# Performance work log

Measured on AMD Instinct MI355X. Metric: run time of the kernel, lower is better.

The kernel has to match this reference:

```python
import jax, jax.numpy as jnp
import numpy as np

B, S, H = 4, 2048, 768
ROUTING_GAIN = 1.0
LN_EPS = 1e-5
MAS_EPS = 1e-9


def _mas_normalize(logits):
    m = jnp.max(jnp.abs(logits), axis=-1, keepdims=True)
    return jax.nn.relu(logits / (m + MAS_EPS))


def _layer_norm(x, w, b):
    mu = jnp.mean(x, axis=-1, keepdims=True)
    var = jnp.var(x, axis=-1, keepdims=True)
    return (x - mu) / jnp.sqrt(var + LN_EPS) * w + b


def _spl(x, proto, gate, mu_w, mu_b):
    # SparseProtoLinear: comp = x @ mu_w.T + mu_b ; match = x @ proto.T / sqrt(d_in) ; gate_logit = x @ gate.T
    scale = 1.0 / jnp.sqrt(jnp.asarray(x.shape[-1], x.dtype))
    match = jnp.einsum('bsd,od->bso', x, proto) * scale
    gate_logit = jnp.einsum('bsd,od->bso', x, gate)
    comp = jnp.einsum('bsd,od->bso', x, mu_w) + mu_b
    return comp, match, gate_logit


def _gate_branch(inp, comp, match, gate_logit):
    routing_logits = (match - _mas_normalize(gate_logit)) * ROUTING_GAIN
    return (inp + comp) * _mas_normalize(routing_logits)


def _rotate_half(x):
    x1, x2 = jnp.split(x, 2, axis=-1)
    return jnp.concatenate([-x2, x1], axis=-1)


def _apply_rope(q, k, cos, sin):
    return q * cos + _rotate_half(q) * sin, k * cos + _rotate_half(k) * sin


def _causal_attention(q, k, v):
    # single-head SDPA over full hidden dim, causal
    d = q.shape[-1]
    scores = jnp.einsum('bqd,bkd->bqk', q, k) / jnp.sqrt(jnp.asarray(d, q.dtype))
    mask = jnp.tril(jnp.ones((q.shape[1], k.shape[1]), dtype=bool))
    scores = jnp.where(mask, scores, jnp.asarray(-jnp.inf, scores.dtype))
    p = jax.nn.softmax(scores, axis=-1)
    return jnp.einsum('bqk,bkd->bqd', p, v)


def setup_inputs() -> dict:
    key = jax.random.key(0)
    ks = iter(jax.random.split(key, 32))
    w_std = 1.0 / np.sqrt(H)
    inp = {'x': jax.random.normal(next(ks), (B, S, H), jnp.float32)}
    # rotary tables: half-dim frequencies duplicated to full hidden dim
    inv_freq = 1.0 / (10000.0 ** (np.arange(0, H, 2, dtype=np.float32) / H))
    ang = np.arange(S, dtype=np.float32)[:, None] * inv_freq[None, :]  # [S, H/2]
    ang = np.concatenate([ang, ang], axis=-1)  # [S, H]
    inp['cos'] = jnp.asarray(np.cos(ang))
    inp['sin'] = jnp.asarray(np.sin(ang))
    inp['ln1_w'] = jnp.ones((H,), jnp.float32)
    inp['ln1_b'] = jnp.zeros((H,), jnp.float32)
    inp['ln2_w'] = jnp.ones((H,), jnp.float32)
    inp['ln2_b'] = jnp.zeros((H,), jnp.float32)
    for name in ['q', 'k', 'v', 'o', 'f1', 'f2']:
        inp[f'{name}_proto'] = jax.random.normal(next(ks), (H, H), jnp.float32) * w_std
        inp[f'{name}_gate'] = jax.random.normal(next(ks), (H, H), jnp.float32) * w_std
        inp[f'{name}_mu_w'] = jax.random.normal(next(ks), (H, H), jnp.float32) * w_std
        inp[f'{name}_mu_b'] = jnp.zeros((H,), jnp.float32)
    return inp


def reference(x, cos, sin, ln1_w, ln1_b, ln2_w, ln2_b,
              q_proto, q_gate, q_mu_w, q_mu_b,
              k_proto, k_gate, k_mu_w, k_mu_b,
              v_proto, v_gate, v_mu_w, v_mu_b,
              o_proto, o_gate, o_mu_w, o_mu_b,
              f1_proto, f1_gate, f1_mu_w, f1_mu_b,
              f2_proto, f2_gate, f2_mu_w, f2_mu_b):
    # prev_protos is None => effective_proto == proto_weight; past_kv is None => causal attention
    ln1_out = _layer_norm(x, ln1_w, ln1_b)
    c_q, mv_q, pc_q = _spl(ln1_out, q_proto, q_gate, q_mu_w, q_mu_b)
    c_k, mv_k, pc_k = _spl(ln1_out, k_proto, k_gate, k_mu_w, k_mu_b)
    c_v, mv_v, pc_v = _spl(ln1_out, v_proto, v_gate, v_mu_w, v_mu_b)
    q = _gate_branch(ln1_out, c_q, mv_q, pc_q)
    k = _gate_branch(ln1_out, c_k, mv_k, pc_k)
    v = _gate_branch(ln1_out, c_v, mv_v, pc_v)
    q, k = _apply_rope(q, k, cos, sin)
    attn_out = _causal_attention(q, k, v)
    c_o, mv_o, pc_o = _spl(attn_out, o_proto, o_gate, o_mu_w, o_mu_b)
    m_o = _gate_branch(attn_out, c_o, mv_o, pc_o)
    x = x + m_o
    ln2_out = _layer_norm(x, ln2_w, ln2_b)
    c1, mv1, pc1 = _spl(ln2_out, f1_proto, f1_gate, f1_mu_w, f1_mu_b)
    h_act = jax.nn.relu(_gate_branch(ln2_out, c1, mv1, pc1))
    c2, mv2, pc2 = _spl(h_act, f2_proto, f2_gate, f2_mu_w, f2_mu_b)
    m2 = _gate_branch(h_act, c2, mv2, pc2)
    x_out = x + m2
    return x_out
```

## Files before the change

kernel.cpp:

```cpp
#include <hip/hip_runtime.h>
#include <hip/hip_bf16.h>
#include <math.h>

#define B_ 4
#define S_ 2048
#define H_ 768
#define M_ (B_*S_)
#define MN ((size_t)M_*(size_t)H_)
#define HH (H_*H_)
#define SS ((size_t)S_*(size_t)S_)
#define SH ((size_t)S_*(size_t)H_)

typedef __bf16 bf16_t;
typedef __bf16 bf16x8 __attribute__((ext_vector_type(8)));
typedef float  f32x4  __attribute__((ext_vector_type(4)));

typedef __attribute__((address_space(3))) void       lds_void_t;
typedef __attribute__((address_space(1))) const void gvoid_t;

template<bool MAXOP>
__device__ __forceinline__ float blockReduce(float v, float* s){
  #pragma unroll
  for (int o = 32; o; o >>= 1){
    float t = __shfl_xor(v, o);
    v = MAXOP ? fmaxf(v, t) : (v + t);
  }
  int lane = threadIdx.x & 63, w = threadIdx.x >> 6;
  if (lane == 0) s[w] = v;
  __syncthreads();
  float r = s[0];
  #pragma unroll
  for (int i = 1; i < 4; i++) r = MAXOP ? fmaxf(r, s[i]) : (r + s[i]);
  __syncthreads();
  return r;
}

struct W18 { const float* p[18]; };

__global__ __launch_bounds__(256) void conv_weights(W18 w, bf16_t* __restrict__ out){
  int m = blockIdx.y;
  int i = blockIdx.x * 256 + threadIdx.x;
  out[(size_t)m * HH + i] = (bf16_t)w.p[m][i];
}

__global__ __launch_bounds__(256) void ln_kernel(const float* __restrict__ x,
                                                 const float* __restrict__ w,
                                                 const float* __restrict__ b,
                                                 bf16_t* __restrict__ outb){
  __shared__ float red[4];
  int row = blockIdx.x, t = threadIdx.x;
  size_t base = (size_t)row * H_;
  float v[3]; float sum = 0.f, sq = 0.f;
  #pragma unroll
  for (int i = 0; i < 3; i++){
    v[i] = x[base + t + i*256];
    sum += v[i]; sq += v[i]*v[i];
  }
  sum = blockReduce<false>(sum, red);
  sq  = blockReduce<false>(sq,  red);
  float mu  = sum * (1.f/H_);
  float var = sq  * (1.f/H_) - mu*mu;
  float rstd = rsqrtf(var + 1e-5f);
  #pragma unroll
  for (int i = 0; i < 3; i++){
    int j = t + i*256;
    outb[base+j] = (bf16_t)((v[i]-mu)*rstd*w[j] + b[j]);
  }
}

__global__ __launch_bounds__(256) void gemm_bt(const bf16_t* __restrict__ A,
                                               const bf16_t* __restrict__ Bm,
                                               bf16_t* __restrict__ C,
                                               int M, int N, int K,
                                               long sA, long sB, long sC,
                                               float scale0, float scale1, float scale2,
                                               const float* __restrict__ bias0, int cmode){
  int gx = gridDim.x, gy = gridDim.y;
  int nwg = gx * gy * gridDim.z;
  int id  = (blockIdx.z * gy + blockIdx.y) * gx + blockIdx.x;
  int sid = (id & 7) * (nwg >> 3) + (id >> 3);
  int bx  = sid % gx;
  int by  = (sid / gx) % gy;
  int z   = sid / (gx * gy);

  A  += (size_t)z * sA;
  Bm += (size_t)z * sB;
  C  += (size_t)z * sC;
  float scale = (z==0) ? scale0 : (z==1) ? scale1 : scale2;
  const float* bias = (z==0) ? bias0 : nullptr;

  int row0 = by * 128, col0 = bx * 128;
  if (cmode == 1 && col0 > row0) return;

  __shared__ bf16_t As[2][128*32];
  __shared__ bf16_t Bs[2][128*32];

  int tid  = threadIdx.x;
  int lane = tid & 63;
  int wave = tid >> 6;
  int wm = wave >> 1, wn = wave & 1;
  int lr = lane & 15, kg = lane >> 4;

  f32x4 acc[4][4] = {};
  int NT = K >> 5;
  if (cmode == 2) { int lim = (row0 + 128) >> 5; NT = NT < lim ? NT : lim; }

  auto stage = [&](int buf, int kt){
    int kk = kt * 32;
    #pragma unroll
    for (int i = 0; i < 2; i++){
      int c  = tid + i*256;
      int r  = c >> 2;
      int c8 = (c & 3) * 8;
      __builtin_amdgcn_global_load_lds((gvoid_t*)(A  + (size_t)(row0 + r)*K + kk + c8),
                                       (lds_void_t*)(&As[buf][c*8]), 16, 0, 0);
      __builtin_amdgcn_global_load_lds((gvoid_t*)(Bm + (size_t)(col0 + r)*K + kk + c8),
                                       (lds_void_t*)(&Bs[buf][c*8]), 16, 0, 0);
    }
  };

  stage(0, 0);
  __syncthreads();
  int buf = 0;
  for (int kt = 0; kt < NT; ++kt){
    if (kt + 1 < NT) stage(buf ^ 1, kt + 1);
    bf16x8 af[4], bfr[4];
    #pragma unroll
    for (int m = 0; m < 4; m++)
      af[m] = *reinterpret_cast<const bf16x8*>(&As[buf][(wm*64 + m*16 + lr)*32 + kg*8]);
    #pragma unroll
    for (int n = 0; n < 4; n++)
      bfr[n] = *reinterpret_cast<const bf16x8*>(&Bs[buf][(wn*64 + n*16 + lr)*32 + kg*8]);
    #pragma unroll
    for (int m = 0; m < 4; m++)
      #pragma unroll
      for (int n = 0; n < 4; n++)
        acc[m][n] = __builtin_amdgcn_mfma_f32_16x16x32_bf16(af[m], bfr[n], acc[m][n], 0, 0, 0);
    __syncthreads();
    buf ^= 1;
  }

  #pragma unroll
  for (int m = 0; m < 4; m++){
    int rb = row0 + wm*64 + m*16 + kg*4;
    #pragma unroll
    for (int n = 0; n < 4; n++){
      int cc = col0 + wn*64 + n*16 + lr;
      float bv = bias ? bias[cc] : 0.f;
      #pragma unroll
      for (int r = 0; r < 4; r++)
        C[(size_t)(rb + r)*N + cc] = (bf16_t)(acc[m][n][r]*scale + bv);
    }
  }
}

__global__ __launch_bounds__(256) void gate_kernel(const bf16_t* __restrict__ inp,
                                                   const bf16_t* __restrict__ c3,
                                                   const float* __restrict__ cosT,
                                                   const float* __restrict__ sinT,
                                                   const float* __restrict__ resid,
                                                   float* __restrict__ outf,
                                                   bf16_t* __restrict__ outb,
                                                   int mode){
  __shared__ float red[4];
  __shared__ float sh[H_];
  int row = blockIdx.x, t = threadIdx.x;
  size_t base = (size_t)row * H_;

  float iv[3], cv[3], mv[3], gv[3];
  float gmax = 0.f;
  #pragma unroll
  for (int i = 0; i < 3; i++){
    int j = t + i*256;
    iv[i] = (float)inp[base + j];
    cv[i] = (float)c3[base + j];
    mv[i] = (float)c3[MN   + base + j];
    gv[i] = (float)c3[2*MN + base + j];
    gmax  = fmaxf(gmax, fabsf(gv[i]));
  }
  gmax = blockReduce<true>(gmax, red);
  float rg = 1.f / (gmax + 1e-9f);

  float rt[3]; float rmax = 0.f;
  #pragma unroll
  for (int i = 0; i < 3; i++){
    float masg = fmaxf(gv[i]*rg, 0.f);
    rt[i] = mv[i] - masg;
    rmax  = fmaxf(rmax, fabsf(rt[i]));
  }
  rmax = blockReduce<true>(rmax, red);
  float rr = 1.f / (rmax + 1e-9f);

  if (mode == 0){
    #pragma unroll
    for (int i = 0; i < 3; i++){
      int j = t + i*256;
      sh[j] = (iv[i] + cv[i]) * fmaxf(rt[i]*rr, 0.f);
    }
    __syncthreads();
    int s = row & (S_ - 1);
    #pragma unroll
    for (int i = 0; i < 3; i++){
      int j = t + i*256;
      float partner = (j < H_/2) ? -sh[j + H_/2] : sh[j - H_/2];
      float o = sh[j]*cosT[(size_t)s*H_ + j] + partner*sinT[(size_t)s*H_ + j];
      outb[base + j] = (bf16_t)o;
    }
  } else {
    #pragma unroll
    for (int i = 0; i < 3; i++){
      int j = t + i*256;
      float val = (iv[i] + cv[i]) * fmaxf(rt[i]*rr, 0.f);
      if (mode == 1)      outb[base + j] = (bf16_t)val;
      else if (mode == 2) outf[base + j] = val + resid[base + j];
      else                outb[base + j] = (bf16_t)fmaxf(val, 0.f);
    }
  }
}

__global__ __launch_bounds__(256) void softmax_causal(const bf16_t* __restrict__ sc,
                                                      bf16_t* __restrict__ P){
  __shared__ float red[4];
  int r = blockIdx.x, b = blockIdx.y, t = threadIdx.x;
  const bf16_t* srow = sc + (size_t)b*SS + (size_t)r * S_;
  bf16_t* prow = P + (size_t)b*SS + (size_t)r * S_;
  int n = r + 1;
  int fill = ((r >> 7) + 1) << 7;
  float m = -1e30f;
  for (int j = t; j < n; j += 256) m = fmaxf(m, (float)srow[j]);
  m = blockReduce<true>(m, red);
  float sum = 0.f;
  for (int j = t; j < n; j += 256) sum += __expf((float)srow[j] - m);
  sum = blockReduce<false>(sum, red);
  float inv = 1.f / sum;
  for (int j = t; j < fill; j += 256)
    prow[j] = (j < n) ? (bf16_t)(__expf((float)srow[j] - m)*inv) : (bf16_t)0.f;
}

__global__ __launch_bounds__(256) void transpose_bf(const bf16_t* __restrict__ in,
                                                    bf16_t* __restrict__ out){
  __shared__ bf16_t tile[32][33];
  int bz = blockIdx.z;
  const bf16_t* I = in  + (size_t)bz * SH;
  bf16_t*       O = out + (size_t)bz * SH;
  int s0 = blockIdx.x*32, h0 = blockIdx.y*32;
  int tx = threadIdx.x, ty = threadIdx.y;
  #pragma unroll
  for (int k = 0; k < 4; k++)
    tile[ty + 8*k][tx] = I[(size_t)(s0 + ty + 8*k)*H_ + h0 + tx];
  __syncthreads();
  #pragma unroll
  for (int k = 0; k < 4; k++)
    O[(size_t)(h0 + ty + 8*k)*S_ + s0 + tx] = tile[tx][ty + 8*k];
}

extern "C" void kernel_launch(void* const* d_in, const int* in_sizes, int n_in,
                              void* d_out, int out_size, void* d_ws, size_t ws_size,
                              hipStream_t stream){
  const float* x    = (const float*)d_in[0];
  const float* cosT = (const float*)d_in[1];
  const float* sinT = (const float*)d_in[2];
  const float* ln1w = (const float*)d_in[3];
  const float* ln1b = (const float*)d_in[4];
  const float* ln2w = (const float*)d_in[5];
  const float* ln2b = (const float*)d_in[6];

  W18 wp; const float* bias[6];
  for (int i = 0; i < 6; i++){
    const float* proto = (const float*)d_in[7 + 4*i + 0];
    const float* gatep = (const float*)d_in[7 + 4*i + 1];
    const float* muw   = (const float*)d_in[7 + 4*i + 2];
    bias[i]            = (const float*)d_in[7 + 4*i + 3];
    wp.p[i*3 + 0] = muw;
    wp.p[i*3 + 1] = proto;
    wp.p[i*3 + 2] = gatep;
  }

  char* w = (char*)d_ws;
  auto alloc = [&](size_t bytes){ void* r = (void*)w; w += (bytes + 255) & ~(size_t)255; return r; };
  bf16_t* w_bf   = (bf16_t*)alloc((size_t)18 * HH * 2);
  bf16_t* a_bf   = (bf16_t*)alloc(MN * 2);
  bf16_t* h_bf   = (bf16_t*)alloc(MN * 2);
  bf16_t* c3b    = (bf16_t*)alloc(3 * MN * 2);
  bf16_t* q_bf   = (bf16_t*)alloc(MN * 2);
  bf16_t* k_bf   = (bf16_t*)alloc(MN * 2);
  bf16_t* v_bf   = (bf16_t*)alloc(MN * 2);
  bf16_t* vt     = (bf16_t*)alloc(MN * 2);
  bf16_t* sc_bf  = (bf16_t*)alloc(B_ * SS * 2);
  bf16_t* p_bf   = (bf16_t*)alloc(B_ * SS * 2);
  bf16_t* attn_b = (bf16_t*)alloc(MN * 2);
  float*  x1     = (float*) alloc(MN * 4);
  (void)ws_size;

  const float rs = 1.0f / sqrtf((float)H_);

  conv_weights<<<dim3(HH/256, 18), 256, 0, stream>>>(wp, w_bf);
  ln_kernel<<<M_, 256, 0, stream>>>(x, ln1w, ln1b, a_bf);

  bf16_t* qkv[3] = {q_bf, k_bf, v_bf};
  for (int s = 0; s < 3; s++){
    gemm_bt<<<dim3(H_/128, M_/128, 3), 256, 0, stream>>>(
        a_bf, w_bf + (size_t)s*3*HH, c3b, M_, H_, H_,
        0, (long)HH, (long)MN, 1.f, rs, 1.f, bias[s], 0);
    gate_kernel<<<M_, 256, 0, stream>>>(a_bf, c3b, cosT, sinT, nullptr, nullptr, qkv[s], (s < 2) ? 0 : 1);
  }

  transpose_bf<<<dim3(S_/32, H_/32, B_), dim3(32, 8), 0, stream>>>(v_bf, vt);

  gemm_bt<<<dim3(S_/128, S_/128, B_), 256, 0, stream>>>(
      q_bf, k_bf, sc_bf, S_, S_, H_,
      (long)SH, (long)SH, (long)SS, rs, rs, rs, nullptr, 1);

  softmax_causal<<<dim3(S_, B_), 256, 0, stream>>>(sc_bf, p_bf);

  gemm_bt<<<dim3(H_/128, S_/128, B_), 256, 0, stream>>>(
      p_bf, vt, attn_b, S_, H_, S_,
      (long)SS, (long)SH, (long)SH, 1.f, 1.f, 1.f, nullptr, 2);

  gemm_bt<<<dim3(H_/128, M_/128, 3), 256, 0, stream>>>(
      attn_b, w_bf + (size_t)9*HH, c3b, M_, H_, H_, 0, (long)HH, (long)MN, 1.f, rs, 1.f, bias[3], 0);
  gate_kernel<<<M_, 256, 0, stream>>>(attn_b, c3b, nullptr, nullptr, x, x1, nullptr, 2);

  ln_kernel<<<M_, 256, 0, stream>>>(x1, ln2w, ln2b, a_bf);

  gemm_bt<<<dim3(H_/128, M_/128, 3), 256, 0, stream>>>(
      a_bf, w_bf + (size_t)12*HH, c3b, M_, H_, H_, 0, (long)HH, (long)MN, 1.f, rs, 1.f, bias[4], 0);
  gate_kernel<<<M_, 256, 0, stream>>>(a_bf, c3b, nullptr, nullptr, nullptr, nullptr, h_bf, 3);

  gemm_bt<<<dim3(H_/128, M_/128, 3), 256, 0, stream>>>(
      h_bf, w_bf + (size_t)15*HH, c3b, M_, H_, H_, 0, (long)HH, (long)MN, 1.f, rs, 1.f, bias[5], 0);
  gate_kernel<<<M_, 256, 0, stream>>>(h_bf, c3b, nullptr, nullptr, x1, (float*)d_out, nullptr, 2);
}
```

Measured before the change: 525.6 us.

## Add 256x256 pipelined GEMM, wave-per-row gate kernel, vectorized weight conversion

Introduces a new 256x256-tile GEMM with 512 threads, 128KB dynamic LDS, swizzled global-to-LDS async loads, double buffering and interleaved MFMA phases. It replaces the 128-tile GEMM for all projection GEMMs and the QK^T score GEMM. The gate kernel is rewritten to give one wavefront per row with vectorized loads, wave shuffles instead of block reductions, and a shuffle-based rotate-half. Weight conversion is vectorized four-wide. Larger tiles raise data reuse but leave fewer workgroups (e.g. 3x32x3 for projections), which can hurt occupancy across the 256 CUs.

```diff
diff --git a/kernel.cpp b/kernel.cpp
--- a/kernel.cpp
+++ b/kernel.cpp
@@ -13,10 +13,16 @@
 
 typedef __bf16 bf16_t;
 typedef __bf16 bf16x8 __attribute__((ext_vector_type(8)));
+typedef __bf16 bf16x4 __attribute__((ext_vector_type(4)));
 typedef float  f32x4  __attribute__((ext_vector_type(4)));
+typedef unsigned short u16;
+typedef u16 u16x4 __attribute__((ext_vector_type(4)));
 
 typedef __attribute__((address_space(3))) void       lds_void_t;
 typedef __attribute__((address_space(1))) const void gvoid_t;
+
+__device__ __forceinline__ float b2f(u16 u){ unsigned x = (unsigned)u << 16; float f; __builtin_memcpy(&f,&x,4); return f; }
+__device__ __forceinline__ u16 f2b(float f){ bf16_t h = (bf16_t)f; u16 u; __builtin_memcpy(&u,&h,2); return u; }
 
 template<bool MAXOP>
 __device__ __forceinline__ float blockReduce(float v, float* s){
@@ -35,12 +41,20 @@
   return r;
 }
 
+__device__ __forceinline__ float waveMax(float v){
+  #pragma unroll
+  for (int o = 1; o < 64; o <<= 1) v = fmaxf(v, __shfl_xor(v, o));
+  return v;
+}
+
 struct W18 { const float* p[18]; };
 
 __global__ __launch_bounds__(256) void conv_weights(W18 w, bf16_t* __restrict__ out){
   int m = blockIdx.y;
-  int i = blockIdx.x * 256 + threadIdx.x;
-  out[(size_t)m * HH + i] = (bf16_t)w.p[m][i];
+  int i = (blockIdx.x * 256 + threadIdx.x) * 4;
+  f32x4 v = *(const f32x4*)(w.p[m] + i);
+  bf16x4 o; o[0]=(bf16_t)v[0]; o[1]=(bf16_t)v[1]; o[2]=(bf16_t)v[2]; o[3]=(bf16_t)v[3];
+  *(bf16x4*)(out + (size_t)m * HH + i) = o;
 }
 
 __global__ __launch_bounds__(256) void ln_kernel(const float* __restrict__ x,
@@ -65,6 +79,144 @@
   for (int i = 0; i < 3; i++){
     int j = t + i*256;
     outb[base+j] = (bf16_t)((v[i]-mu)*rstd*w[j] + b[j]);
+  }
+}
+
+__global__ __launch_bounds__(512, 2) void gemm256(const bf16_t* __restrict__ A,
+                                                  const bf16_t* __restrict__ Bm,
+                                                  bf16_t* __restrict__ C,
+                                                  int M, int N, int K,
+                                                  long sA, long sB, long sC,
+                                                  float scale0, float scale1, float scale2,
+                                                  const float* __restrict__ bias0, int causal){
+  extern __shared__ char smem[];
+  char* Abase = smem;
+  char* Bbase = smem + 65536;
+
+  int gx = gridDim.x, gy = gridDim.y;
+  int nwg = gx * gy * gridDim.z;
+  int id  = (blockIdx.z * gy + blockIdx.y) * gx + blockIdx.x;
+  int sid = (id & 7) * (nwg >> 3) + (id >> 3);
+  int bx  = sid % gx;
+  int by  = (sid / gx) % gy;
+  int z   = sid / (gx * gy);
+
+  A  += (size_t)z * sA;
+  Bm += (size_t)z * sB;
+  C  += (size_t)z * sC;
+  float scale = (z==0) ? scale0 : (z==1) ? scale1 : scale2;
+  const float* bias = (z==0) ? bias0 : nullptr;
+
+  int row0 = by * 256, col0 = bx * 256;
+  if (causal && col0 > row0) return;
+
+  int tid  = threadIdx.x;
+  int lane = tid & 63, wid = tid >> 6;
+  int wm = wid >> 2, wn = wid & 3;
+  int lr = lane & 15, kg = lane >> 4;
+
+  int NT = K >> 6;
+
+  int r1 = tid >> 3, cb = tid & 7;
+  int ecol = (cb ^ (r1 & 7)) * 8;
+
+  auto stageA = [&](int buf, int h, int kt){
+    const bf16_t* src = A + (size_t)(row0 + h*128 + r1) * K + kt*64 + ecol;
+    char* dst = Abase + buf*32768 + (h*128 + r1)*128 + cb*16;
+    __builtin_amdgcn_global_load_lds((gvoid_t*)src,          (lds_void_t*)dst,          16, 0, 0);
+    __builtin_amdgcn_global_load_lds((gvoid_t*)(src + (size_t)64*K), (lds_void_t*)(dst + 64*128), 16, 0, 0);
+  };
+  auto stageB = [&](int buf, int h, int kt){
+    const bf16_t* src = Bm + (size_t)(col0 + h*128 + r1) * K + kt*64 + ecol;
+    char* dst = Bbase + buf*32768 + (h*128 + r1)*128 + cb*16;
+    __builtin_amdgcn_global_load_lds((gvoid_t*)src,          (lds_void_t*)dst,          16, 0, 0);
+    __builtin_amdgcn_global_load_lds((gvoid_t*)(src + (size_t)64*K), (lds_void_t*)(dst + 64*128), 16, 0, 0);
+  };
+  auto rdA = [&](int buf, int r, int s) -> bf16x8 {
+    int off = r*128 + ((s*64 + kg*16) ^ ((r & 7) << 4));
+    return *(const bf16x8*)(Abase + buf*32768 + off);
+  };
+  auto rdB = [&](int buf, int r, int s) -> bf16x8 {
+    int off = r*128 + ((s*64 + kg*16) ^ ((r & 7) << 4));
+    return *(const bf16x8*)(Bbase + buf*32768 + off);
+  };
+
+  f32x4 acc[8][4] = {};
+
+  stageA(0,0,0); stageA(0,1,0); stageB(0,0,0); stageB(0,1,0);
+  if (NT > 1){ stageA(1,0,1); stageA(1,1,1); }
+  asm volatile("s_waitcnt vmcnt(4)" ::: "memory");
+  __builtin_amdgcn_s_barrier();
+
+  bf16x8 a0[8], a1[8], b0[4], b1[4];
+  for (int t = 0; t < NT; ++t){
+    int buf = t & 1, nb = buf ^ 1;
+    #pragma unroll
+    for (int m = 0; m < 8; m++) a0[m] = rdA(buf, wm*128 + m*16 + lr, 0);
+    #pragma unroll
+    for (int n = 0; n < 4; n++) b0[n] = rdB(buf, wn*64 + n*16 + lr, 0);
+    if (t + 1 < NT) stageB(nb, 0, t+1);
+    __builtin_amdgcn_s_barrier();
+    __builtin_amdgcn_s_setprio(1);
+    #pragma unroll
+    for (int m = 0; m < 8; m++){
+      acc[m][0] = __builtin_amdgcn_mfma_f32_16x16x32_bf16(a0[m], b0[0], acc[m][0], 0,0,0);
+      acc[m][1] = __builtin_amdgcn_mfma_f32_16x16x32_bf16(a0[m], b0[1], acc[m][1], 0,0,0);
+    }
+    __builtin_amdgcn_s_setprio(0);
+    __builtin_amdgcn_s_barrier();
+    #pragma unroll
+    for (int m = 0; m < 8; m++) a1[m] = rdA(buf, wm*128 + m*16 + lr, 1);
+    #pragma unroll
+    for (int n = 0; n < 4; n++) b1[n] = rdB(buf, wn*64 + n*16 + lr, 1);
+    if (t + 1 < NT) stageB(nb, 1, t+1);
+    __builtin_amdgcn_s_barrier();
+    __builtin_amdgcn_s_setprio(1);
+    #pragma unroll
+    for (int m = 0; m < 8; m++){
+      acc[m][2] = __builtin_amdgcn_mfma_f32_16x16x32_bf16(a0[m], b0[2], acc[m][2], 0,0,0);
+      acc[m][3] = __builtin_amdgcn_mfma_f32_16x16x32_bf16(a0[m], b0[3], acc[m][3], 0,0,0);
+    }
+    __builtin_amdgcn_s_setprio(0);
+    asm volatile("s_waitcnt lgkmcnt(0)" ::: "memory");
+    __builtin_amdgcn_s_barrier();
+    if (t + 2 < NT) stageA(buf, 0, t+2);
+    __builtin_amdgcn_s_barrier();
+    __builtin_amdgcn_s_setprio(1);
+    #pragma unroll
+    for (int m = 0; m < 8; m++){
+      acc[m][0] = __builtin_amdgcn_mfma_f32_16x16x32_bf16(a1[m], b1[0], acc[m][0], 0,0,0);
+      acc[m][1] = __builtin_amdgcn_mfma_f32_16x16x32_bf16(a1[m], b1[1], acc[m][1], 0,0,0);
+    }
+    __builtin_amdgcn_s_setprio(0);
+    __builtin_amdgcn_s_barrier();
+    if (t + 2 < NT) stageA(buf, 1, t+2);
+    __builtin_amdgcn_s_barrier();
+    __builtin_amdgcn_s_setprio(1);
+    #pragma unroll
+    for (int m = 0; m < 8; m++){
+      acc[m][2] = __builtin_amdgcn_mfma_f32_16x16x32_bf16(a1[m], b1[2], acc[m][2], 0,0,0);
+      acc[m][3] = __builtin_amdgcn_mfma_f32_16x16x32_bf16(a1[m], b1[3], acc[m][3], 0,0,0);
+    }
+    __builtin_amdgcn_s_setprio(0);
+    if (t + 1 < NT){
+      if (t + 2 < NT) asm volatile("s_waitcnt vmcnt(4)" ::: "memory");
+      else            asm volatile("s_waitcnt vmcnt(0)" ::: "memory");
+      __builtin_amdgcn_s_barrier();
+    }
+  }
+
+  #pragma unroll
+  for (int m = 0; m < 8; m++){
+    int rb = row0 + wm*128 + m*16 + kg*4;
+    #pragma unroll
+    for (int n = 0; n < 4; n++){
+      int cc = col0 + wn*64 + n*16 + lr;
+      float bv = bias ? bias[cc] : 0.f;
+      #pragma unroll
+      for (int r = 0; r < 4; r++)
+        C[(size_t)(rb + r)*N + cc] = (bf16_t)(acc[m][n][r]*scale + bv);
+    }
   }
 }
 
@@ -162,58 +314,86 @@
                                                    float* __restrict__ outf,
                                                    bf16_t* __restrict__ outb,
                                                    int mode){
-  __shared__ float red[4];
-  __shared__ float sh[H_];
-  int row = blockIdx.x, t = threadIdx.x;
-  size_t base = (size_t)row * H_;
-
-  float iv[3], cv[3], mv[3], gv[3];
+  int wid = threadIdx.x >> 6, l = threadIdx.x & 63;
+  int row = blockIdx.x * 4 + wid;
+  size_t base = (size_t)row * H_ + l*12;
+
+  float iv[12], cv[12], mv[12], gv[12];
+  #pragma unroll
+  for (int i = 0; i < 3; i++){
+    u16x4 a = *(const u16x4*)(inp + base + 4*i);
+    u16x4 b = *(const u16x4*)(c3  + base + 4*i);
+    u16x4 c = *(const u16x4*)(c3 + MN   + base + 4*i);
+    u16x4 d = *(const u16x4*)(c3 + 2*MN + base + 4*i);
+    #pragma unroll
+    for (int j = 0; j < 4; j++){
+      iv[4*i+j] = b2f(a[j]); cv[4*i+j] = b2f(b[j]);
+      mv[4*i+j] = b2f(c[j]); gv[4*i+j] = b2f(d[j]);
+    }
+  }
   float gmax = 0.f;
   #pragma unroll
-  for (int i = 0; i < 3; i++){
-    int j = t + i*256;
-    iv[i] = (float)inp[base + j];
-    cv[i] = (float)c3[base + j];
-    mv[i] = (float)c3[MN   + base + j];
-    gv[i] = (float)c3[2*MN + base + j];
-    gmax  = fmaxf(gmax, fabsf(gv[i]));
-  }
-  gmax = blockReduce<true>(gmax, red);
+  for (int j = 0; j < 12; j++) gmax = fmaxf(gmax, fabsf(gv[j]));
+  gmax = waveMax(gmax);
   float rg = 1.f / (gmax + 1e-9f);
 
-  float rt[3]; float rmax = 0.f;
-  #pragma unroll
-  for (int i = 0; i < 3; i++){
-    float masg = fmaxf(gv[i]*rg, 0.f);
-    rt[i] = mv[i] - masg;
-    rmax  = fmaxf(rmax, fabsf(rt[i]));
-  }
-  rmax = blockReduce<true>(rmax, red);
+  float rt[12], rmax = 0.f;
+  #pragma unroll
+  for (int j = 0; j < 12; j++){
+    rt[j] = mv[j] - fmaxf(gv[j]*rg, 0.f);
+    rmax  = fmaxf(rmax, fabsf(rt[j]));
+  }
+  rmax = waveMax(rmax);
   float rr = 1.f / (rmax + 1e-9f);
 
+  float val[12];
+  #pragma unroll
+  for (int j = 0; j < 12; j++) val[j] = (iv[j] + cv[j]) * fmaxf(rt[j]*rr, 0.f);
+
   if (mode == 0){
+    int s = row & (S_ - 1);
+    const float* cp = cosT + (size_t)s*H_ + l*12;
+    const float* sp = sinT + (size_t)s*H_ + l*12;
+    float o[12];
     #pragma unroll
     for (int i = 0; i < 3; i++){
-      int j = t + i*256;
-      sh[j] = (iv[i] + cv[i]) * fmaxf(rt[i]*rr, 0.f);
-    }
-    __syncthreads();
-    int s = row & (S_ - 1);
+      f32x4 cw = *(const f32x4*)(cp + 4*i);
+      f32x4 sw = *(const f32x4*)(sp + 4*i);
+      #pragma unroll
+      for (int j = 0; j < 4; j++){
+        int q = 4*i + j;
+        float partner = __shfl_xor(val[q], 32);
+        if (l < 32) partner = -partner;
+        o[q] = val[q]*cw[j] + partner*sw[j];
+      }
+    }
     #pragma unroll
     for (int i = 0; i < 3; i++){
-      int j = t + i*256;
-      float partner = (j < H_/2) ? -sh[j + H_/2] : sh[j - H_/2];
-      float o = sh[j]*cosT[(size_t)s*H_ + j] + partner*sinT[(size_t)s*H_ + j];
-      outb[base + j] = (bf16_t)o;
+      u16x4 u; 
+      #pragma unroll
+      for (int j = 0; j < 4; j++) u[j] = f2b(o[4*i+j]);
+      *(u16x4*)(outb + base + 4*i) = u;
+    }
+  } else if (mode == 1 || mode == 3){
+    #pragma unroll
+    for (int i = 0; i < 3; i++){
+      u16x4 u;
+      #pragma unroll
+      for (int j = 0; j < 4; j++){
+        float v = val[4*i+j];
+        if (mode == 3) v = fmaxf(v, 0.f);
+        u[j] = f2b(v);
+      }
+      *(u16x4*)(outb + base + 4*i) = u;
     }
   } else {
     #pragma unroll
     for (int i = 0; i < 3; i++){
-      int j = t + i*256;
-      float val = (iv[i] + cv[i]) * fmaxf(rt[i]*rr, 0.f);
-      if (mode == 1)      outb[base + j] = (bf16_t)val;
-      else if (mode == 2) outf[base + j] = val + resid[base + j];
-      else                outb[base + j] = (bf16_t)fmaxf(val, 0.f);
+      f32x4 rv = *(const f32x4*)(resid + base + 4*i);
+      f32x4 ov;
+      #pragma unroll
+      for (int j = 0; j < 4; j++) ov[j] = val[4*i+j] + rv[j];
+      *(f32x4*)(outf + base + 4*i) = ov;
     }
   }
 }
@@ -276,6 +456,8 @@
     wp.p[i*3 + 2] = gatep;
   }
 
+  hipFuncSetAttribute((const void*)gemm256, hipFuncAttributeMaxDynamicSharedMemorySize, 131072);
+
   char* w = (char*)d_ws;
   auto alloc = [&](size_t bytes){ void* r = (void*)w; w += (bytes + 255) & ~(size_t)255; return r; };
   bf16_t* w_bf   = (bf16_t*)alloc((size_t)18 * HH * 2);
@@ -294,20 +476,20 @@
 
   const float rs = 1.0f / sqrtf((float)H_);
 
-  conv_weights<<<dim3(HH/256, 18), 256, 0, stream>>>(wp, w_bf);
+  conv_weights<<<dim3(HH/1024, 18), 256, 0, stream>>>(wp, w_bf);
   ln_kernel<<<M_, 256, 0, stream>>>(x, ln1w, ln1b, a_bf);
 
   bf16_t* qkv[3] = {q_bf, k_bf, v_bf};
   for (int s = 0; s < 3; s++){
-    gemm_bt<<<dim3(H_/128, M_/128, 3), 256, 0, stream>>>(
+    gemm256<<<dim3(H_/256, M_/256, 3), 512, 131072, stream>>>(
         a_bf, w_bf + (size_t)s*3*HH, c3b, M_, H_, H_,
         0, (long)HH, (long)MN, 1.f, rs, 1.f, bias[s], 0);
-    gate_kernel<<<M_, 256, 0, stream>>>(a_bf, c3b, cosT, sinT, nullptr, nullptr, qkv[s], (s < 2) ? 0 : 1);
+    gate_kernel<<<M_/4, 256, 0, stream>>>(a_bf, c3b, cosT, sinT, nullptr, nullptr, qkv[s], (s < 2) ? 0 : 1);
   }
 
   transpose_bf<<<dim3(S_/32, H_/32, B_), dim3(32, 8), 0, stream>>>(v_bf, vt);
 
-  gemm_bt<<<dim3(S_/128, S_/128, B_), 256, 0, stream>>>(
+  gemm256<<<dim3(S_/256, S_/256, B_), 512, 131072, stream>>>(
       q_bf, k_bf, sc_bf, S_, S_, H_,
       (long)SH, (long)SH, (long)SS, rs, rs, rs, nullptr, 1);
 
@@ -317,17 +499,17 @@
       p_bf, vt, attn_b, S_, H_, S_,
       (long)SS, (long)SH, (long)SH, 1.f, 1.f, 1.f, nullptr, 2);
 
-  gemm_bt<<<dim3(H_/128, M_/128, 3), 256, 0, stream>>>(
+  gemm256<<<dim3(H_/256, M_/256, 3), 512, 131072, stream>>>(
       attn_b, w_bf + (size_t)9*HH, c3b, M_, H_, H_, 0, (long)HH, (long)MN, 1.f, rs, 1.f, bias[3], 0);
-  gate_kernel<<<M_, 256, 0, stream>>>(attn_b, c3b, nullptr, nullptr, x, x1, nullptr, 2);
+  gate_kernel<<<M_/4, 256, 0, stream>>>(attn_b, c3b, nullptr, nullptr, x, x1, nullptr, 2);
 
   ln_kernel<<<M_, 256, 0, stream>>>(x1, ln2w, ln2b, a_bf);
 
-  gemm_bt<<<dim3(H_/128, M_/128, 3), 256, 0, stream>>>(
+  gemm256<<<dim3(H_/256, M_/256, 3), 512, 131072, stream>>>(
       a_bf, w_bf + (size_t)12*HH, c3b, M_, H_, H_, 0, (long)HH, (long)MN, 1.f, rs, 1.f, bias[4], 0);
-  gate_kernel<<<M_, 256, 0, stream>>>(a_bf, c3b, nullptr, nullptr, nullptr, nullptr, h_bf, 3);
-
-  gemm_bt<<<dim3(H_/128, M_/128, 3), 256, 0, stream>>>(
+  gate_kernel<<<M_/4, 256, 0, stream>>>(a_bf, c3b, nullptr, nullptr, nullptr, nullptr, h_bf, 3);
+
+  gemm256<<<dim3(H_/256, M_/256, 3), 512, 131072, stream>>>(
       h_bf, w_bf + (size_t)15*HH, c3b, M_, H_, H_, 0, (long)HH, (long)MN, 1.f, rs, 1.f, bias[5], 0);
-  gate_kernel<<<M_, 256, 0, stream>>>(h_bf, c3b, nullptr, nullptr, x1, (float*)d_out, nullptr, 2);
-}
+  gate_kernel<<<M_/4, 256, 0, stream>>>(h_bf, c3b, nullptr, nullptr, x1, (float*)d_out, nullptr, 2);
+}
```

Result: slower. 550.1 us (+4.7%).
